# Performance work log

Hardware: AMD Instinct MI355X
Metric: run time of the kernel (lower is better)

## Reference

```python
import jax, jax.numpy as jnp
import numpy as np

B, S, E, H, FF = 4, 2048, 1024, 16, 4096
TD = 32  # transition_dim


def _layer_norm(v, g, b, eps=1e-5):
    m = v.mean(-1, keepdims=True)
    var = ((v - m) ** 2).mean(-1, keepdims=True)
    return (v - m) * jax.lax.rsqrt(var + eps) * g + b


def setup_inputs() -> dict:
    key = jax.random.key(0)
    ks = jax.random.split(key, 8)
    w = 0.02
    return {
        "x": jax.random.normal(ks[0], (B, S, E), dtype=jnp.float32),
        "transition_dim": TD,
        "ln1_g": jnp.ones((E,), jnp.float32),
        "ln1_b": jnp.zeros((E,), jnp.float32),
        "ln2_g": jnp.ones((E,), jnp.float32),
        "ln2_b": jnp.zeros((E,), jnp.float32),
        "w_qkv": jax.random.normal(ks[1], (3 * E, E), jnp.float32) * w,
        "b_qkv": jnp.zeros((3 * E,), jnp.float32),
        "w_o": jax.random.normal(ks[2], (E, E), jnp.float32) * w,
        "b_o": jnp.zeros((E,), jnp.float32),
        "w_fc1": jax.random.normal(ks[3], (FF, E), jnp.float32) * w,
        "b_fc1": jnp.zeros((FF,), jnp.float32),
        "w_fc2": jax.random.normal(ks[4], (E, FF), jnp.float32) * w,
        "b_fc2": jnp.zeros((E,), jnp.float32),
    }


def reference(x, transition_dim, ln1_g, ln1_b, ln2_g, ln2_b, w_qkv, b_qkv,
              w_o, b_o, w_fc1, b_fc1, w_fc2, b_fc2):
    Bx, Sx, Ex = x.shape
    Dh = Ex // H
    xn = _layer_norm(x, ln1_g, ln1_b)
    qkv = xn @ w_qkv.T + b_qkv                      # [B,S,3E]
    q, k, v = jnp.split(qkv, 3, axis=-1)
    def heads(t):
        return t.reshape(Bx, Sx, H, Dh).transpose(0, 2, 1, 3)  # [B,H,S,Dh]
    q, k, v = heads(q), heads(k), heads(v)
    scores = jnp.einsum("bhqd,bhkd->bhqk", q, k) / np.sqrt(Dh).astype(np.float32)
    # custom mask: causal (j > i) OR periodic value-column (j % TD == TD-1) blocked
    i = jnp.arange(Sx)
    mask = (i[None, :] > i[:, None]) | ((i[None, :] % transition_dim) == transition_dim - 1)
    scores = jnp.where(mask[None, None], -jnp.inf, scores)
    p = jax.nn.softmax(scores, axis=-1)
    attn = jnp.einsum("bhqk,bhkd->bhqd", p, v)
    attn = attn.transpose(0, 2, 1, 3).reshape(Bx, Sx, Ex)
    attn = attn @ w_o.T + b_o
    x = x + attn
    h = _layer_norm(x, ln2_g, ln2_b)
    h = jax.nn.gelu(h @ w_fc1.T + b_fc1, approximate=False) @ w_fc2.T + b_fc2
    return x + h
```

## Files before the change

### kernel.cpp

```cpp
#include <hip/hip_runtime.h>
#include <hip/hip_bf16.h>

typedef unsigned short u16;
typedef unsigned int u32;
typedef short bf16x8 __attribute__((ext_vector_type(8)));
typedef float f32x4 __attribute__((ext_vector_type(4)));
typedef float f32x16 __attribute__((ext_vector_type(16)));

#define B_ 4
#define S_ 2048
#define E_ 1024
#define H_ 16
#define FF_ 4096
#define M_ 8192

__device__ __forceinline__ u16 f2bf(float f) {
    u32 u = __float_as_uint(f);
    u32 r = (u + 0x7FFFu + ((u >> 16) & 1u)) >> 16;
    return (u16)r;
}
__device__ __forceinline__ float bf2f(u16 v) {
    return __uint_as_float(((u32)v) << 16);
}
__device__ __forceinline__ u32 cvtpk(float lo, float hi) {
    u32 r;
    asm("v_cvt_pk_bf16_f32 %0, %1, %2" : "=v"(r) : "v"(lo), "v"(hi));
    return r;
}
__device__ __forceinline__ void pswap(u32& a, u32& b) {
    asm("v_permlane32_swap_b32 %0, %1" : "+v"(a), "+v"(b));
}
__device__ __forceinline__ void gload16(const void* g, void* l) {
    __builtin_amdgcn_global_load_lds(
        (__attribute__((address_space(1))) void*)g,
        (__attribute__((address_space(3))) void*)l, 16, 0, 0);
}

__global__ __launch_bounds__(256) void cvt4_kernel(const float* __restrict__ s0, u16* __restrict__ d0,
                                                   const float* __restrict__ s1, u16* __restrict__ d1,
                                                   const float* __restrict__ s2, u16* __restrict__ d2,
                                                   const float* __restrict__ s3, u16* __restrict__ d3) {
    int blk = blockIdx.x;
    const float* s; u16* d; int base;
    if (blk < 3072)      { s = s0; d = d0; base = blk; }
    else if (blk < 4096) { s = s1; d = d1; base = blk - 3072; }
    else if (blk < 8192) { s = s2; d = d2; base = blk - 4096; }
    else                 { s = s3; d = d3; base = blk - 8192; }
    int i = base * 256 + threadIdx.x;
    float4 v = ((const float4*)s)[i];
    ushort4 o;
    o.x = f2bf(v.x); o.y = f2bf(v.y); o.z = f2bf(v.z); o.w = f2bf(v.w);
    ((ushort4*)d)[i] = o;
}

__global__ __launch_bounds__(256) void vtrans_kernel(const u16* __restrict__ qkv,
                                                     u16* __restrict__ vt) {
    __shared__ u16 tile[64 * 67];
    int t = threadIdx.x;
    int st = blockIdx.x;
    int bh = blockIdx.y;
    int b = bh >> 4, h = bh & 15;
    int s0 = st * 64;
    int r = t >> 3, c0 = (t & 7) * 8;
#pragma unroll
    for (int half = 0; half < 2; half++) {
        int rr = r + half * 32;
        const u16* src = qkv + (size_t)(b * S_ + s0 + rr) * 3072 + 2048 + h * 64 + c0;
        uint4 v = *(const uint4*)src;
        u16* pv = (u16*)&v;
#pragma unroll
        for (int e = 0; e < 8; e++) tile[(c0 + e) * 67 + rr] = pv[e];
    }
    __syncthreads();
    int d = t >> 2, ch = t & 3;
    u16 buf[16];
#pragma unroll
    for (int j = 0; j < 16; j++) buf[j] = tile[d * 67 + ch * 16 + j];
    u16* dst = vt + ((size_t)bh * 64 + d) * 2048 + s0 + ch * 16;
    *(uint4*)dst = *(uint4*)&buf[0];
    *(uint4*)(dst + 8) = *(uint4*)&buf[8];
}

__global__ __launch_bounds__(256) void ln_kernel(const float* __restrict__ x,
                                                 const float* __restrict__ g,
                                                 const float* __restrict__ bb,
                                                 u16* __restrict__ out) {
    int row = blockIdx.x;
    int t = threadIdx.x;
    const float4* xr = (const float4*)(x + (size_t)row * E_);
    float4 v = xr[t];
    float s = v.x + v.y + v.z + v.w;
    float sq = v.x * v.x + v.y * v.y + v.z * v.z + v.w * v.w;
    for (int o = 1; o < 64; o <<= 1) {
        s += __shfl_xor(s, o, 64);
        sq += __shfl_xor(sq, o, 64);
    }
    __shared__ float ss[4], sqs[4];
    int w = t >> 6, l = t & 63;
    if (l == 0) { ss[w] = s; sqs[w] = sq; }
    __syncthreads();
    s = ss[0] + ss[1] + ss[2] + ss[3];
    sq = sqs[0] + sqs[1] + sqs[2] + sqs[3];
    float mean = s * (1.0f / E_);
    float var = sq * (1.0f / E_) - mean * mean;
    float rstd = rsqrtf(var + 1e-5f);
    float4 gv = ((const float4*)g)[t];
    float4 bv = ((const float4*)bb)[t];
    ushort4 o4;
    o4.x = f2bf((v.x - mean) * rstd * gv.x + bv.x);
    o4.y = f2bf((v.y - mean) * rstd * gv.y + bv.y);
    o4.z = f2bf((v.z - mean) * rstd * gv.z + bv.z);
    o4.w = f2bf((v.w - mean) * rstd * gv.w + bv.w);
    ((ushort4*)(out + (size_t)row * E_))[t] = o4;
}

template <int EPI>
__global__ __launch_bounds__(256) void gemm128(const u16* __restrict__ A,
                                               const u16* __restrict__ Bt,
                                               const float* __restrict__ bias,
                                               void* __restrict__ outp,
                                               const float* __restrict__ resid,
                                               int N, int K) {
    __shared__ u16 ldsA[2 * 8192];
    __shared__ u16 ldsB[2 * 8192];
    int t = threadIdx.x;
    int wid = t >> 6, l = t & 63, l15 = l & 15, hi4 = l >> 4;
    int wm = wid >> 1, wn = wid & 1;

    int nwg = gridDim.x;
    int flat = blockIdx.x;
    int swz = (flat & 7) * (nwg >> 3) + (flat >> 3);
    int nx = N >> 7;
    int m0 = (swz / nx) * 128, n0 = (swz % nx) * 128;
    const size_t Kb = (size_t)K * 2;

    f32x4 acc[4][4];
    f32x4 zf = {0.f, 0.f, 0.f, 0.f};
#pragma unroll
    for (int i = 0; i < 4; i++)
#pragma unroll
        for (int j = 0; j < 4; j++) acc[i][j] = zf;

    auto stageA = [&](int buf, int k0) {
#pragma unroll
        for (int rr = 0; rr < 4; ++rr) {
            int o = t * 16 + rr * 4096;
            int lr = o >> 7;
            int gch = ((o >> 4) & 7) ^ (lr & 7);
            gload16((const char*)A + (size_t)(m0 + lr) * Kb + k0 * 2 + gch * 16,
                    (char*)ldsA + buf * 16384 + o);
        }
    };
    auto stageB = [&](int buf, int k0) {
#pragma unroll
        for (int rr = 0; rr < 4; ++rr) {
            int o = t * 16 + rr * 4096;
            int lr = o >> 7;
            int gch = ((o >> 4) & 7) ^ (lr & 7);
            gload16((const char*)Bt + (size_t)(n0 + lr) * Kb + k0 * 2 + gch * 16,
                    (char*)ldsB + buf * 16384 + o);
        }
    };

    int NT = K >> 6;
    stageA(0, 0); stageB(0, 0);
    stageA(1, 64); stageB(1, 64);

    for (int tt = 0; tt < NT; ++tt) {
        int c = tt & 1;
        asm volatile("s_waitcnt vmcnt(8)" ::: "memory");
        __builtin_amdgcn_sched_barrier(0);
        __builtin_amdgcn_s_barrier();

        bf16x8 af[4][2], bf[4][2];
#pragma unroll
        for (int mi = 0; mi < 4; mi++)
#pragma unroll
            for (int ks = 0; ks < 2; ks++) {
                int lr = wm * 64 + mi * 16 + l15;
                int ob = lr * 128 + ks * 64 + hi4 * 16;
                af[mi][ks] = *(const bf16x8*)((const char*)ldsA + c * 16384 +
                                              (ob ^ ((lr & 7) << 4)));
            }
#pragma unroll
        for (int nq = 0; nq < 4; nq++)
#pragma unroll
            for (int ks = 0; ks < 2; ks++) {
                int lr = wn * 64 + nq * 16 + l15;
                int ob = lr * 128 + ks * 64 + hi4 * 16;
                bf[nq][ks] = *(const bf16x8*)((const char*)ldsB + c * 16384 +
                                              (ob ^ ((lr & 7) << 4)));
            }
        asm volatile("s_waitcnt lgkmcnt(0)" ::: "memory");
        __builtin_amdgcn_sched_barrier(0);
        __builtin_amdgcn_s_setprio(1);
#pragma unroll
        for (int mi = 0; mi < 4; mi++)
#pragma unroll
            for (int nq = 0; nq < 4; nq++)
#pragma unroll
                for (int ks = 0; ks < 2; ks++)
                    acc[mi][nq] = __builtin_amdgcn_mfma_f32_16x16x32_bf16(
                        af[mi][ks], bf[nq][ks], acc[mi][nq], 0, 0, 0);
        __builtin_amdgcn_s_setprio(0);
        __builtin_amdgcn_s_barrier();

        int kn = (tt + 2) * 64; if (kn >= K) kn = 0;
        stageA(c, kn); stageB(c, kn);
    }
    asm volatile("s_waitcnt vmcnt(0)" ::: "memory");
    __builtin_amdgcn_sched_barrier(0);

    float bias_v[4];
#pragma unroll
    for (int nq = 0; nq < 4; nq++) bias_v[nq] = bias[n0 + wn * 64 + nq * 16 + l15];

#pragma unroll
    for (int mi = 0; mi < 4; mi++)
#pragma unroll
        for (int nq = 0; nq < 4; nq++)
#pragma unroll
            for (int j = 0; j < 4; j++) {
                int row = m0 + wm * 64 + mi * 16 + hi4 * 4 + j;
                int col = n0 + wn * 64 + nq * 16 + l15;
                float v = acc[mi][nq][j] + bias_v[nq];
                size_t idx = (size_t)row * N + col;
                if (EPI == 2) v = 0.5f * v * (1.0f + erff(v * 0.70710678118f));
                if (EPI == 1)
                    ((float*)outp)[idx] = resid[idx] + v;
                else
                    ((u16*)outp)[idx] = f2bf(v);
            }
}

template <int EPI>
__global__ __launch_bounds__(512, 2) void gemm256n128(const u16* __restrict__ A,
                                                      const u16* __restrict__ Bt,
                                                      const float* __restrict__ bias,
                                                      void* __restrict__ outp,
                                                      const float* __restrict__ resid,
                                                      int N, int K) {
    __shared__ u16 ldsA[2 * 2 * 8192];
    __shared__ u16 ldsB[2 * 8192];
    int t = threadIdx.x;
    int wid = t >> 6, l = t & 63, l15 = l & 15, hi4 = l >> 4;
    int wm = wid >> 2, wn = wid & 3;

    int nwg = gridDim.x;
    int flat = blockIdx.x;
    int swz = (flat & 7) * (nwg >> 3) + (flat >> 3);
    int nx = N >> 7;
    int m0 = (swz / nx) * 256, n0 = (swz % nx) * 128;
    const size_t Kb = (size_t)K * 2;

    f32x4 acc[8][2];
    f32x4 zf = {0.f, 0.f, 0.f, 0.f};
#pragma unroll
    for (int i = 0; i < 8; i++)
#pragma unroll
        for (int j = 0; j < 2; j++) acc[i][j] = zf;

    auto stageA = [&](int buf, int h, int k0) {
#pragma unroll
        for (int rr = 0; rr < 2; ++rr) {
            int o = t * 16 + rr * 8192;
            int lr = o >> 7;
            int gch = ((o >> 4) & 7) ^ (lr & 7);
            int grow = m0 + (lr >> 6) * 128 + h * 64 + (lr & 63);
            gload16((const char*)A + (size_t)grow * Kb + k0 * 2 + gch * 16,
                    (char*)ldsA + (buf * 2 + h) * 16384 + o);
        }
    };
    auto stageB = [&](int buf, int k0) {
#pragma unroll
        for (int rr = 0; rr < 2; ++rr) {
            int o = t * 16 + rr * 8192;
            int lr = o >> 7;
            int gch = ((o >> 4) & 7) ^ (lr & 7);
            int grow = n0 + lr;
            gload16((const char*)Bt + (size_t)grow * Kb + k0 * 2 + gch * 16,
                    (char*)ldsB + buf * 16384 + o);
        }
    };

    auto readA = [&](int bq, int mh, bf16x8 (&af)[4][2]) {
#pragma unroll
        for (int mi = 0; mi < 4; mi++)
#pragma unroll
            for (int ks = 0; ks < 2; ks++) {
                int lr = wm * 64 + mi * 16 + l15;
                int ob = lr * 128 + ks * 64 + hi4 * 16;
                af[mi][ks] = *(const bf16x8*)((const char*)ldsA +
                             (bq * 2 + mh) * 16384 + (ob ^ ((lr & 7) << 4)));
            }
    };
    auto readB = [&](int bq, bf16x8 (&bfr)[2][2]) {
#pragma unroll
        for (int nq = 0; nq < 2; nq++)
#pragma unroll
            for (int ks = 0; ks < 2; ks++) {
                int lr = wn * 32 + nq * 16 + l15;
                int ob = lr * 128 + ks * 64 + hi4 * 16;
                bfr[nq][ks] = *(const bf16x8*)((const char*)ldsB +
                              bq * 16384 + (ob ^ ((lr & 7) << 4)));
            }
    };
    auto mma = [&](bf16x8 (&af)[4][2], bf16x8 (&bfr)[2][2], int mh) {
#pragma unroll
        for (int mi = 0; mi < 4; mi++)
#pragma unroll
            for (int nq = 0; nq < 2; nq++)
#pragma unroll
                for (int ks = 0; ks < 2; ks++)
                    acc[mh * 4 + mi][nq] =
                        __builtin_amdgcn_mfma_f32_16x16x32_bf16(
                            af[mi][ks], bfr[nq][ks], acc[mh * 4 + mi][nq], 0, 0, 0);
    };

#define GWAIT(N)                                            \
    asm volatile("s_waitcnt vmcnt(" #N ")" ::: "memory");   \
    __builtin_amdgcn_sched_barrier(0);
#define PH_MID                                              \
    __builtin_amdgcn_s_barrier();                           \
    asm volatile("s_waitcnt lgkmcnt(0)" ::: "memory");      \
    __builtin_amdgcn_sched_barrier(0);                      \
    __builtin_amdgcn_s_setprio(1);
#define PH_END                                              \
    __builtin_amdgcn_s_setprio(0);                          \
    __builtin_amdgcn_s_barrier();

    int ITERS = K >> 7;
    stageB(0, 0); stageA(0, 0, 0); stageA(0, 1, 0);
    stageB(1, 64); stageA(1, 0, 64);
    GWAIT(4);
    __builtin_amdgcn_s_barrier();
    for (int s = 0; s < ITERS; ++s) {
        int k1 = (2 * s + 1) << 6;
        int k2 = (2 * s + 2) << 6; if (k2 >= K) k2 = 0;
        int k3 = (2 * s + 3) << 6; if (k3 >= K) k3 = 0;
        bf16x8 af[4][2], br[2][2];
        readA(0, 0, af); readB(0, br); stageA(1, 1, k1);
        PH_MID; mma(af, br, 0); PH_END;
        readA(0, 1, af); stageB(0, k2); stageA(0, 0, k2); GWAIT(4);
        PH_MID; mma(af, br, 1); PH_END;
        readA(1, 0, af); readB(1, br); stageA(0, 1, k2);
        PH_MID; mma(af, br, 0); PH_END;
        readA(1, 1, af); stageB(1, k3); stageA(1, 0, k3); GWAIT(4);
        PH_MID; mma(af, br, 1); PH_END;
    }
#undef GWAIT
#undef PH_MID
#undef PH_END

    float bias_v[2];
#pragma unroll
    for (int nq = 0; nq < 2; nq++) bias_v[nq] = bias[n0 + wn * 32 + nq * 16 + l15];

#pragma unroll
    for (int mf = 0; mf < 8; mf++)
#pragma unroll
        for (int nq = 0; nq < 2; nq++)
#pragma unroll
            for (int j = 0; j < 4; j++) {
                int row = m0 + wm * 128 + mf * 16 + hi4 * 4 + j;
                int col = n0 + wn * 32 + nq * 16 + l15;
                float v = acc[mf][nq][j] + bias_v[nq];
                size_t idx = (size_t)row * N + col;
                if (EPI == 2) v = 0.5f * v * (1.0f + erff(v * 0.70710678118f));
                if (EPI == 1)
                    ((float*)outp)[idx] = resid[idx] + v;
                else
                    ((u16*)outp)[idx] = f2bf(v);
            }
}

__global__ __launch_bounds__(128) void attn_kernel(const u16* __restrict__ qkv,
                                                   const u16* __restrict__ vt,
                                                   u16* __restrict__ aout) {
    __shared__ u16 Ksb[2 * 4096];
    __shared__ u16 Vsb[2 * 4096];
    int t = threadIdx.x;
    int wv = t >> 6, l = t & 63;
    int q31 = l & 31, hi = l >> 5;
    int flat = blockIdx.x;
    int logical = (flat & 7) * 128 + (flat >> 3);
    int bh = logical >> 4, p0 = logical & 15;
    int b = bh >> 4, h = bh & 15;

    const float qs = 0.18033688011f;
    const float THR = 44.3616f;

    const char* srcK0 = (const char*)(qkv + E_ + (size_t)(b * S_ + (t >> 3)) * 3072 + h * 64) +
                        ((t & 7) ^ ((t >> 3) & 7)) * 16;
    const char* srcV0 = (const char*)(vt + ((size_t)(bh * 64 + (t >> 3))) * 2048) +
                        ((t & 7) ^ ((t >> 3) & 7)) * 16;
    auto issueK = [&](int buf, int j0) {
#pragma unroll
        for (int pp = 0; pp < 4; pp++)
            gload16(srcK0 + (size_t)pp * 98304 + (size_t)j0 * 6144,
                    (char*)Ksb + buf * 8192 + 16 * t + 2048 * pp);
    };
    auto issueV = [&](int buf, int j0) {
#pragma unroll
        for (int pp = 0; pp < 4; pp++)
            gload16(srcV0 + (size_t)pp * 65536 + (size_t)j0 * 2,
                    (char*)Vsb + buf * 8192 + 16 * t + 2048 * pp);
    };

    f32x16 zf16;
#pragma unroll
    for (int r = 0; r < 16; r++) zf16[r] = 0.f;

    for (int half = 0; half < 2; ++half) {
        int qt = half ? (31 - p0) : p0;
        int rowq = qt * 64 + wv * 32 + q31;

        bf16x8 qreg[4];
        const u16* qbase = qkv + (size_t)(b * S_ + rowq) * 3072 + h * 64 + hi * 8;
#pragma unroll
        for (int g = 0; g < 4; g++) qreg[g] = *(const bf16x8*)(qbase + 16 * g);

        f32x16 o0 = zf16, o1 = zf16;
        float mrun = -INFINITY, lrun = 0.f;

        int j1 = (qt >= 1) ? 64 : 0;
        issueK(0, 0); issueV(0, 0);
        issueK(1, j1); issueV(1, j1);

        for (int jt = 0; jt <= qt; ++jt) {
            int cur = jt & 1;
            int j0 = jt * 64;
            asm volatile("s_waitcnt vmcnt(8)" ::: "memory");
            __builtin_amdgcn_sched_barrier(0);
            __builtin_amdgcn_s_barrier();

            const u16* Kc = Ksb + cur * 4096;
            const u16* Vc = Vsb + cur * 4096;

            f32x16 s0 = zf16, s1 = zf16;
            __builtin_amdgcn_s_setprio(1);
#pragma unroll
            for (int g = 0; g < 4; g++) {
                int r0 = q31, r1 = 32 + q31;
                bf16x8 k0 = *(const bf16x8*)&Kc[((r0 << 6) + hi * 8 + 16 * g) ^ ((r0 & 7) << 3)];
                bf16x8 k1 = *(const bf16x8*)&Kc[((r1 << 6) + hi * 8 + 16 * g) ^ ((r1 & 7) << 3)];
                s0 = __builtin_amdgcn_mfma_f32_32x32x16_bf16(k0, qreg[g], s0, 0, 0, 0);
                s1 = __builtin_amdgcn_mfma_f32_32x32x16_bf16(k1, qreg[g], s1, 0, 0, 0);
            }
            __builtin_amdgcn_s_setprio(0);

            float mx = -INFINITY;
            int cb0 = j0 + 4 * hi;
            if (jt == qt) {
#pragma unroll
                for (int r = 0; r < 16; r++) {
                    const int cc = (r & 3) + 8 * (r >> 2);
                    float v0 = s0[r], v1 = s1[r];
                    bool bad0 = (cb0 + cc > rowq) || (r == 15 && hi);
                    bool bad1 = (cb0 + 32 + cc > rowq) || (r == 15 && hi);
                    v0 = bad0 ? -INFINITY : v0;
                    v1 = bad1 ? -INFINITY : v1;
                    s0[r] = v0; s1[r] = v1;
                    mx = fmaxf(mx, fmaxf(v0, v1));
                }
            } else {
#pragma unroll
                for (int r = 0; r < 16; r++) {
                    float v0 = s0[r], v1 = s1[r];
                    if (r == 15) {
                        v0 = hi ? -INFINITY : v0;
                        v1 = hi ? -INFINITY : v1;
                        s0[r] = v0; s1[r] = v1;
                    }
                    mx = fmaxf(mx, fmaxf(v0, v1));
                }
            }
            mx = fmaxf(mx, __shfl_xor(mx, 32, 64));

            bool dokeep = __all(mx <= mrun + THR);
            if (!dokeep) {
                float mnew = fmaxf(mrun, mx);
                float sc = __builtin_amdgcn_exp2f((mrun - mnew) * qs);
#pragma unroll
                for (int r = 0; r < 16; r++) { o0[r] *= sc; o1[r] *= sc; }
                lrun *= sc;
                mrun = mnew;
            }
            float mq = mrun * qs;

            float sa = 0.f, sb = 0.f, sc2 = 0.f, sd = 0.f;
#pragma unroll
            for (int r = 0; r < 16; r++) {
                float p0 = __builtin_amdgcn_exp2f(fmaf(s0[r], qs, -mq));
                float p1 = __builtin_amdgcn_exp2f(fmaf(s1[r], qs, -mq));
                s0[r] = p0; s1[r] = p1;
                if (r & 1) { sb += p0; sd += p1; } else { sa += p0; sc2 += p1; }
            }
            lrun += (sa + sb) + (sc2 + sd);

            bf16x8 pa[4];
#pragma unroll
            for (int g = 0; g < 4; g++) {
                const int bs = (g & 1) * 8;
                u32 wa, wb, wc, wd;
                if (g < 2) {
                    wa = cvtpk(s0[bs + 0], s0[bs + 1]);
                    wb = cvtpk(s0[bs + 4], s0[bs + 5]);
                    wc = cvtpk(s0[bs + 2], s0[bs + 3]);
                    wd = cvtpk(s0[bs + 6], s0[bs + 7]);
                } else {
                    wa = cvtpk(s1[bs + 0], s1[bs + 1]);
                    wb = cvtpk(s1[bs + 4], s1[bs + 5]);
                    wc = cvtpk(s1[bs + 2], s1[bs + 3]);
                    wd = cvtpk(s1[bs + 6], s1[bs + 7]);
                }
                pswap(wa, wb);
                pswap(wc, wd);
                union { u32 w[4]; bf16x8 f; } u;
                u.w[0] = wa; u.w[1] = wc; u.w[2] = wb; u.w[3] = wd;
                pa[g] = u.f;
            }

            __builtin_amdgcn_s_setprio(1);
#pragma unroll
            for (int g = 0; g < 4; g++) {
                int d0 = q31, d1 = 32 + q31;
                bf16x8 v0 = *(const bf16x8*)&Vc[((d0 << 6) + hi * 8 + 16 * g) ^ ((d0 & 7) << 3)];
                bf16x8 v1 = *(const bf16x8*)&Vc[((d1 << 6) + hi * 8 + 16 * g) ^ ((d1 & 7) << 3)];
                o0 = __builtin_amdgcn_mfma_f32_32x32x16_bf16(v0, pa[g], o0, 0, 0, 0);
                o1 = __builtin_amdgcn_mfma_f32_32x32x16_bf16(v1, pa[g], o1, 0, 0, 0);
            }
            __builtin_amdgcn_s_setprio(0);

            __builtin_amdgcn_s_barrier();
            int nj = (jt + 2 <= qt) ? (jt + 2) * 64 : 0;
            issueK(cur, nj);
            issueV(cur, nj);
        }

        lrun += __shfl_xor(lrun, 32, 64);
        float inv = 1.0f / lrun;
        u16* orow = aout + (size_t)(b * S_ + rowq) * E_ + h * 64 + 4 * hi;
#pragma unroll
        for (int r = 0; r < 16; r++) {
            const int cc = (r & 3) + 8 * (r >> 2);
            orow[cc] = f2bf(o0[r] * inv);
            orow[32 + cc] = f2bf(o1[r] * inv);
        }

        if (half == 0) {
            asm volatile("s_waitcnt vmcnt(0)" ::: "memory");
            __builtin_amdgcn_sched_barrier(0);
            __builtin_amdgcn_s_barrier();
        }
    }
}

extern "C" void kernel_launch(void* const* d_in, const int* in_sizes, int n_in,
                              void* d_out, int out_size, void* d_ws, size_t ws_size,
                              hipStream_t stream) {
    const float* x = (const float*)d_in[0];
    const float* ln1_g = (const float*)d_in[2];
    const float* ln1_b = (const float*)d_in[3];
    const float* ln2_g = (const float*)d_in[4];
    const float* ln2_b = (const float*)d_in[5];
    const float* w_qkv = (const float*)d_in[6];
    const float* b_qkv = (const float*)d_in[7];
    const float* w_o = (const float*)d_in[8];
    const float* b_o = (const float*)d_in[9];
    const float* w_fc1 = (const float*)d_in[10];
    const float* b_fc1 = (const float*)d_in[11];
    const float* w_fc2 = (const float*)d_in[12];
    const float* b_fc2 = (const float*)d_in[13];
    float* out = (float*)d_out;
    char* ws = (char*)d_ws;

    u16* wqkv_bf = (u16*)(ws);
    u16* wo_bf   = (u16*)(ws + 6291456);
    u16* wfc1_bf = (u16*)(ws + 8388608);
    u16* wfc2_bf = (u16*)(ws + 16777216);
    u16* xn_bf   = (u16*)(ws + 25165824);
    u16* qkv_bf  = (u16*)(ws + 41943040);
    u16* ffn1_bf = (u16*)(ws + 41943040);
    u16* attn_bf = (u16*)(ws + 92274688);
    float* x2    = (float*)(ws + 109051904);
    u16* vtw     = (u16*)(ws + 109051904);
    (void)in_sizes; (void)n_in; (void)out_size; (void)ws_size;

    cvt4_kernel<<<12288, 256, 0, stream>>>(w_qkv, wqkv_bf, w_o, wo_bf,
                                           w_fc1, wfc1_bf, w_fc2, wfc2_bf);

    ln_kernel<<<M_, 256, 0, stream>>>(x, ln1_g, ln1_b, xn_bf);

    gemm128<0><<<1536, 256, 0, stream>>>(xn_bf, wqkv_bf, b_qkv, qkv_bf, nullptr, 3072, 1024);

    vtrans_kernel<<<dim3(32, 64), 256, 0, stream>>>(qkv_bf, vtw);

    attn_kernel<<<1024, 128, 0, stream>>>(qkv_bf, vtw, attn_bf);

    gemm256n128<1><<<256, 512, 0, stream>>>(attn_bf, wo_bf, b_o, x2, x, 1024, 1024);

    ln_kernel<<<M_, 256, 0, stream>>>(x2, ln2_g, ln2_b, xn_bf);

    gemm128<2><<<2048, 256, 0, stream>>>(xn_bf, wfc1_bf, b_fc1, ffn1_bf, nullptr, 4096, 1024);

    gemm256n128<1><<<256, 512, 0, stream>>>(ffn1_bf, wfc2_bf, b_fc2, out, x2, 1024, 4096);
}
```

Baseline: 393.3 us.

## Replace 128x128 GEMM with 256x256-tile 8-wave pipelined kernel for QKV and FC1

Replaces the 128x128-tile, 4-wave GEMM used for the QKV projection and FC1 with a 256x256-tile, 8-wave kernel. It uses split half-tile LDS staging and a four-phase software pipeline like the existing gemm256n128. Larger tiles double reuse of each loaded A/B tile and cut global/L2 traffic per FLOP. The cost is 64KB of LDS and more accumulator registers per block. Grids shrink to 384 and 512 blocks, which risks tail imbalance on the GPU's CUs.

```diff
diff --git a/kernel.cpp b/kernel.cpp
--- a/kernel.cpp
+++ b/kernel.cpp
@@ -115,121 +115,151 @@
 }
 
 template <int EPI>
-__global__ __launch_bounds__(256) void gemm128(const u16* __restrict__ A,
-                                               const u16* __restrict__ Bt,
-                                               const float* __restrict__ bias,
-                                               void* __restrict__ outp,
-                                               const float* __restrict__ resid,
-                                               int N, int K) {
-    __shared__ u16 ldsA[2 * 8192];
-    __shared__ u16 ldsB[2 * 8192];
+__global__ __launch_bounds__(512, 2) void gemm256m(const u16* __restrict__ A,
+                                                   const u16* __restrict__ Bt,
+                                                   const float* __restrict__ bias,
+                                                   void* __restrict__ outp,
+                                                   int N, int K) {
+    __shared__ u16 ldsA[2 * 2 * 8192];
+    __shared__ u16 ldsB[2 * 2 * 8192];
     int t = threadIdx.x;
     int wid = t >> 6, l = t & 63, l15 = l & 15, hi4 = l >> 4;
-    int wm = wid >> 1, wn = wid & 1;
+    int wm = wid >> 2, wn = wid & 3;
 
     int nwg = gridDim.x;
     int flat = blockIdx.x;
     int swz = (flat & 7) * (nwg >> 3) + (flat >> 3);
-    int nx = N >> 7;
-    int m0 = (swz / nx) * 128, n0 = (swz % nx) * 128;
+    int nx = N >> 8;
+    int m0 = (swz / nx) * 256, n0 = (swz % nx) * 256;
     const size_t Kb = (size_t)K * 2;
 
-    f32x4 acc[4][4];
+    f32x4 acc[8][4];
     f32x4 zf = {0.f, 0.f, 0.f, 0.f};
 #pragma unroll
-    for (int i = 0; i < 4; i++)
+    for (int i = 0; i < 8; i++)
 #pragma unroll
         for (int j = 0; j < 4; j++) acc[i][j] = zf;
 
-    auto stageA = [&](int buf, int k0) {
-#pragma unroll
-        for (int rr = 0; rr < 4; ++rr) {
-            int o = t * 16 + rr * 4096;
+    auto stageA = [&](int buf, int h, int k0) {
+#pragma unroll
+        for (int rr = 0; rr < 2; ++rr) {
+            int o = t * 16 + rr * 8192;
             int lr = o >> 7;
             int gch = ((o >> 4) & 7) ^ (lr & 7);
-            gload16((const char*)A + (size_t)(m0 + lr) * Kb + k0 * 2 + gch * 16,
-                    (char*)ldsA + buf * 16384 + o);
+            int grow = m0 + (lr >> 6) * 128 + h * 64 + (lr & 63);
+            gload16((const char*)A + (size_t)grow * Kb + k0 * 2 + gch * 16,
+                    (char*)ldsA + (buf * 2 + h) * 16384 + o);
         }
     };
-    auto stageB = [&](int buf, int k0) {
-#pragma unroll
-        for (int rr = 0; rr < 4; ++rr) {
-            int o = t * 16 + rr * 4096;
+    auto stageB = [&](int buf, int h, int k0) {
+#pragma unroll
+        for (int rr = 0; rr < 2; ++rr) {
+            int o = t * 16 + rr * 8192;
             int lr = o >> 7;
             int gch = ((o >> 4) & 7) ^ (lr & 7);
-            gload16((const char*)Bt + (size_t)(n0 + lr) * Kb + k0 * 2 + gch * 16,
-                    (char*)ldsB + buf * 16384 + o);
+            int grow = n0 + (lr >> 5) * 64 + h * 32 + (lr & 31);
+            gload16((const char*)Bt + (size_t)grow * Kb + k0 * 2 + gch * 16,
+                    (char*)ldsB + (buf * 2 + h) * 16384 + o);
         }
     };
 
-    int NT = K >> 6;
-    stageA(0, 0); stageB(0, 0);
-    stageA(1, 64); stageB(1, 64);
-
-    for (int tt = 0; tt < NT; ++tt) {
-        int c = tt & 1;
-        asm volatile("s_waitcnt vmcnt(8)" ::: "memory");
-        __builtin_amdgcn_sched_barrier(0);
-        __builtin_amdgcn_s_barrier();
-
-        bf16x8 af[4][2], bf[4][2];
+    auto readA = [&](int bq, int mh, bf16x8 (&af)[4][2]) {
 #pragma unroll
         for (int mi = 0; mi < 4; mi++)
 #pragma unroll
             for (int ks = 0; ks < 2; ks++) {
                 int lr = wm * 64 + mi * 16 + l15;
                 int ob = lr * 128 + ks * 64 + hi4 * 16;
-                af[mi][ks] = *(const bf16x8*)((const char*)ldsA + c * 16384 +
-                                              (ob ^ ((lr & 7) << 4)));
-            }
-#pragma unroll
-        for (int nq = 0; nq < 4; nq++)
+                af[mi][ks] = *(const bf16x8*)((const char*)ldsA +
+                             (bq * 2 + mh) * 16384 + (ob ^ ((lr & 7) << 4)));
+            }
+    };
+    auto readB = [&](int bq, int nh, bf16x8 (&bfr)[2][2]) {
+#pragma unroll
+        for (int nq = 0; nq < 2; nq++)
 #pragma unroll
             for (int ks = 0; ks < 2; ks++) {
-                int lr = wn * 64 + nq * 16 + l15;
+                int lr = wn * 32 + nq * 16 + l15;
                 int ob = lr * 128 + ks * 64 + hi4 * 16;
-                bf[nq][ks] = *(const bf16x8*)((const char*)ldsB + c * 16384 +
-                                              (ob ^ ((lr & 7) << 4)));
-            }
-        asm volatile("s_waitcnt lgkmcnt(0)" ::: "memory");
-        __builtin_amdgcn_sched_barrier(0);
-        __builtin_amdgcn_s_setprio(1);
+                bfr[nq][ks] = *(const bf16x8*)((const char*)ldsB +
+                              (bq * 2 + nh) * 16384 + (ob ^ ((lr & 7) << 4)));
+            }
+    };
+    auto mma = [&](bf16x8 (&af)[4][2], bf16x8 (&bfr)[2][2], int mh, int nh) {
 #pragma unroll
         for (int mi = 0; mi < 4; mi++)
 #pragma unroll
-            for (int nq = 0; nq < 4; nq++)
+            for (int nq = 0; nq < 2; nq++)
 #pragma unroll
                 for (int ks = 0; ks < 2; ks++)
-                    acc[mi][nq] = __builtin_amdgcn_mfma_f32_16x16x32_bf16(
-                        af[mi][ks], bf[nq][ks], acc[mi][nq], 0, 0, 0);
+                    acc[mh * 4 + mi][nh * 2 + nq] =
+                        __builtin_amdgcn_mfma_f32_16x16x32_bf16(
+                            af[mi][ks], bfr[nq][ks], acc[mh * 4 + mi][nh * 2 + nq], 0, 0, 0);
+    };
+
+#define GWAIT(N)                                            \
+    asm volatile("s_waitcnt vmcnt(" #N ")" ::: "memory");   \
+    __builtin_amdgcn_sched_barrier(0);
+#define PH_MID                                              \
+    __builtin_amdgcn_s_barrier();                           \
+    asm volatile("s_waitcnt lgkmcnt(0)" ::: "memory");      \
+    __builtin_amdgcn_sched_barrier(0);                      \
+    __builtin_amdgcn_s_setprio(1);
+#define PH_END                                              \
+    __builtin_amdgcn_s_setprio(0);                          \
+    __builtin_amdgcn_s_barrier();
+
+    int ITERS = K >> 7;
+    stageB(0, 0, 0); stageB(0, 1, 0); stageA(0, 0, 0); stageA(0, 1, 0);
+    stageB(1, 0, 64); stageB(1, 1, 64); stageA(1, 0, 64);
+    GWAIT(6);
+    __builtin_amdgcn_s_barrier();
+    for (int s = 0; s < ITERS; ++s) {
+        int k1 = (2 * s + 1) << 6;
+        int k2 = (2 * s + 2) << 6; if (k2 >= K) k2 = 0;
+        int k3 = (2 * s + 3) << 6; if (k3 >= K) k3 = 0;
+        bf16x8 af[4][2], b0[2][2], b1[2][2];
+        readA(0, 0, af); readB(0, 0, b0); readB(0, 1, b1);
+        stageA(1, 1, k1);
+        PH_MID; mma(af, b0, 0, 0); mma(af, b1, 0, 1); PH_END;
+        readA(0, 1, af);
+        stageB(0, 0, k2); stageB(0, 1, k2); stageA(0, 0, k2);
+        PH_MID; mma(af, b0, 1, 0); mma(af, b1, 1, 1);
         __builtin_amdgcn_s_setprio(0);
+        GWAIT(8);
         __builtin_amdgcn_s_barrier();
-
-        int kn = (tt + 2) * 64; if (kn >= K) kn = 0;
-        stageA(c, kn); stageB(c, kn);
+        readA(1, 0, af); readB(1, 0, b0); readB(1, 1, b1);
+        stageA(0, 1, k2);
+        PH_MID; mma(af, b0, 0, 0); mma(af, b1, 0, 1);
+        __builtin_amdgcn_s_setprio(0);
+        GWAIT(8);
+        __builtin_amdgcn_s_barrier();
+        readA(1, 1, af);
+        stageB(1, 0, k3); stageB(1, 1, k3); stageA(1, 0, k3);
+        GWAIT(6);
+        PH_MID; mma(af, b0, 1, 0); mma(af, b1, 1, 1); PH_END;
     }
-    asm volatile("s_waitcnt vmcnt(0)" ::: "memory");
-    __builtin_amdgcn_sched_barrier(0);
+    GWAIT(0);
+#undef GWAIT
+#undef PH_MID
+#undef PH_END
 
     float bias_v[4];
 #pragma unroll
-    for (int nq = 0; nq < 4; nq++) bias_v[nq] = bias[n0 + wn * 64 + nq * 16 + l15];
-
-#pragma unroll
-    for (int mi = 0; mi < 4; mi++)
-#pragma unroll
-        for (int nq = 0; nq < 4; nq++)
+    for (int nf = 0; nf < 4; nf++) bias_v[nf] = bias[n0 + wn * 64 + nf * 16 + l15];
+
+#pragma unroll
+    for (int mf = 0; mf < 8; mf++)
+#pragma unroll
+        for (int nf = 0; nf < 4; nf++)
 #pragma unroll
             for (int j = 0; j < 4; j++) {
-                int row = m0 + wm * 64 + mi * 16 + hi4 * 4 + j;
-                int col = n0 + wn * 64 + nq * 16 + l15;
-                float v = acc[mi][nq][j] + bias_v[nq];
+                int row = m0 + wm * 128 + mf * 16 + hi4 * 4 + j;
+                int col = n0 + wn * 64 + nf * 16 + l15;
+                float v = acc[mf][nf][j] + bias_v[nf];
                 size_t idx = (size_t)row * N + col;
                 if (EPI == 2) v = 0.5f * v * (1.0f + erff(v * 0.70710678118f));
-                if (EPI == 1)
-                    ((float*)outp)[idx] = resid[idx] + v;
-                else
-                    ((u16*)outp)[idx] = f2bf(v);
+                ((u16*)outp)[idx] = f2bf(v);
             }
 }
 
@@ -348,6 +378,7 @@
         readA(1, 1, af); stageB(1, k3); stageA(1, 0, k3); GWAIT(4);
         PH_MID; mma(af, br, 1); PH_END;
     }
+    GWAIT(0);
 #undef GWAIT
 #undef PH_MID
 #undef PH_END
@@ -366,7 +397,6 @@
                 int col = n0 + wn * 32 + nq * 16 + l15;
                 float v = acc[mf][nq][j] + bias_v[nq];
                 size_t idx = (size_t)row * N + col;
-                if (EPI == 2) v = 0.5f * v * (1.0f + erff(v * 0.70710678118f));
                 if (EPI == 1)
                     ((float*)outp)[idx] = resid[idx] + v;
                 else
@@ -592,7 +622,7 @@
 
     ln_kernel<<<M_, 256, 0, stream>>>(x, ln1_g, ln1_b, xn_bf);
 
-    gemm128<0><<<1536, 256, 0, stream>>>(xn_bf, wqkv_bf, b_qkv, qkv_bf, nullptr, 3072, 1024);
+    gemm256m<0><<<384, 512, 0, stream>>>(xn_bf, wqkv_bf, b_qkv, qkv_bf, 3072, 1024);
 
     vtrans_kernel<<<dim3(32, 64), 256, 0, stream>>>(qkv_bf, vtw);
 
@@ -602,7 +632,7 @@
 
     ln_kernel<<<M_, 256, 0, stream>>>(x2, ln2_g, ln2_b, xn_bf);
 
-    gemm128<2><<<2048, 256, 0, stream>>>(xn_bf, wfc1_bf, b_fc1, ffn1_bf, nullptr, 4096, 1024);
+    gemm256m<2><<<512, 512, 0, stream>>>(xn_bf, wfc1_bf, b_fc1, ffn1_bf, 4096, 1024);
 
     gemm256n128<1><<<256, 512, 0, stream>>>(ffn1_bf, wfc2_bf, b_fc2, out, x2, 1024, 4096);
 }
```

Result: faster. 381.5 us (-3.0%).
